# Performance work log

Measured on AMD Instinct MI355X. Metric: run time of the kernel, lower is better.

Reference implementation:

```python
import jax, jax.numpy as jnp
from jax import lax
import numpy as np

B, NW, L, E, H, V = 8192, 4, 16, 128, 128, 64  # batch, words/example, max chars, emsize, hidden, char vocab


def setup_inputs() -> dict:
    key = jax.random.key(0)
    ks = jax.random.split(key, 13)
    s = 0.05
    return {
        "word_ids": jax.random.randint(ks[0], (B, NW, L), 0, V, dtype=jnp.int32),
        "lengths": jax.random.randint(ks[1], (B, NW), 1, L + 1, dtype=jnp.int32),
        "emb_i": jax.random.normal(ks[2], (V, E), jnp.float32),
        "W_ih": jax.random.normal(ks[3], (4 * H, E), jnp.float32) * s,
        "W_hh": jax.random.normal(ks[4], (4 * H, H), jnp.float32) * s,
        "b_ih": jax.random.normal(ks[5], (4 * H,), jnp.float32) * s,
        "b_hh": jax.random.normal(ks[6], (4 * H,), jnp.float32) * s,
        "conv1_w": jax.random.normal(ks[7], (4, 1, 2, 2), jnp.float32) * 0.5,
        "conv1_b": jax.random.normal(ks[8], (4,), jnp.float32) * 0.1,
        "conv2_w": jax.random.normal(ks[9], (8, 4, 2, 2), jnp.float32) * 0.5,
        "conv2_b": jax.random.normal(ks[10], (8,), jnp.float32) * 0.1,
        "scorer_w": jax.random.normal(ks[11], (1, 2 * 2 * 8), jnp.float32) * 0.2,
        "scorer_b": jax.random.normal(ks[12], (1,), jnp.float32) * 0.1,
    }


def reference(word_ids, lengths, emb_i, W_ih, W_hh, b_ih, b_hh,
              conv1_w, conv1_b, conv2_w, conv2_b, scorer_w, scorer_b):
    Bx, NWx, Lx = word_ids.shape
    Hh = W_hh.shape[1]
    BN = Bx * NWx
    # char embeddings for all words, packed: [L, BN, E]
    xs = emb_i[word_ids.reshape(BN, Lx)].transpose(1, 0, 2)
    # ragged lengths -> per-step update mask [L, BN]
    mask = jnp.arange(Lx, dtype=lengths.dtype)[:, None] < lengths.reshape(-1)[None, :]
    h0 = jnp.zeros((BN, Hh), emb_i.dtype)

    def step(carry, xm):
        h, c = carry
        x_t, m = xm
        gates = x_t @ W_ih.T + b_ih + h @ W_hh.T + b_hh  # torch LSTMCell gate order i,f,g,o
        i, f, g, o = jnp.split(gates, 4, axis=-1)
        i = jax.nn.sigmoid(i); f = jax.nn.sigmoid(f)
        g = jnp.tanh(g); o = jax.nn.sigmoid(o)
        c_new = f * c + i * g
        h_new = o * jnp.tanh(c_new)
        m = m[:, None]
        return (jnp.where(m, h_new, h), jnp.where(m, c_new, c)), None

    (h, c), _ = lax.scan(step, (h0, h0), (xs, mask))
    # Model.encode returns the cell state c
    reps = c.reshape(Bx, NWx, Hh)

    # pairwise cosine similarity matrix [B, NW, NW]
    norms = jnp.sqrt(jnp.sum(reps * reps, axis=-1))
    dots = jnp.einsum('bih,bjh->bij', reps, reps)
    cos = dots / (norms[:, :, None] * norms[:, None, :])

    # tiny 2-layer CNN scorer on the NWxNW matrix (NCHW)
    dn = ('NCHW', 'OIHW', 'NCHW')
    x_img = cos[:, None, :, :]
    out = jax.nn.relu(lax.conv_general_dilated(x_img, conv1_w, (1, 1), 'VALID', dimension_numbers=dn)
                      + conv1_b[None, :, None, None])
    out = jax.nn.relu(lax.conv_general_dilated(out, conv2_w, (1, 1), 'VALID', dimension_numbers=dn)
                      + conv2_b[None, :, None, None])
    flat = out.reshape(Bx, -1)  # channel-major flatten matches torch .view
    score = flat @ scorer_w.T + scorer_b
    return jax.nn.sigmoid(score)  # [B, 1] discriminator prob
```

## Files before the change

kernel.cpp:

```cpp
#include <hip/hip_runtime.h>

#define BSZ    8192
#define NWRD   4
#define SEQL   16
#define HDIM   128
#define NSEQ   (BSZ * NWRD)
#define WGSEQ  32
#define UPB    80
#define BINCAP (UPB * WGSEQ)
#define NUNITS (16 * UPB)
#define HSTRIDE 136

typedef float  f32x4  __attribute__((ext_vector_type(4)));
typedef float  f32x16 __attribute__((ext_vector_type(16)));
typedef __bf16 bf16x8 __attribute__((ext_vector_type(8)));

union AccU { f32x16 v; f32x4 q[4]; float f[16]; };

__device__ __forceinline__ unsigned short f2bf(float f) {
    unsigned int u = __builtin_bit_cast(unsigned int, f);
    return (unsigned short)((u + 0x7fff + ((u >> 16) & 1)) >> 16);
}
__device__ __forceinline__ float sigm(float x) {
    return __builtin_amdgcn_rcpf(1.f + __builtin_amdgcn_exp2f(x * -1.44269504f));
}
__device__ __forceinline__ float tanhx(float x) {
    return 1.f - 2.f * __builtin_amdgcn_rcpf(1.f + __builtin_amdgcn_exp2f(x * 2.88539008f));
}

__global__ void prep4(const float* __restrict__ emb, const float* __restrict__ W_ih,
                      const float* __restrict__ b_ih, const float* __restrict__ b_hh,
                      const float* __restrict__ W_hh, const int* __restrict__ lengths,
                      float* __restrict__ P2T, unsigned short* __restrict__ WA,
                      int* __restrict__ perm, int* __restrict__ gh)
{
    __shared__ int lh[16], gbase[16];
    const int blk = blockIdx.x, tid = threadIdx.x;

    if (blk < 128) {
        int idx = blk * 256 + tid;
        int v = idx >> 9, g = (idx >> 7) & 3, j = idx & 127;
        int n = g * 128 + j;
        const f32x4* er = (const f32x4*)(emb  + v * 128);
        const f32x4* wr = (const f32x4*)(W_ih + n * 128);
        f32x4 s4 = er[0] * wr[0];
#pragma unroll
        for (int e = 1; e < 32; ++e) s4 += er[e] * wr[e];
        P2T[idx] = s4.x + s4.y + s4.z + s4.w + b_ih[n] + b_hh[n];
    } else if (blk < 384) {
        int idx = (blk - 128) * 256 + tid;
        int jj = idx & 7, lane = (idx >> 3) & 63, kc = (idx >> 9) & 7, tt = idx >> 12;
        int wv = tt >> 2, g = tt & 3;
        int n = g * 128 + wv * 32 + (lane & 31);
        int k = kc * 16 + (lane >> 5) * 8 + jj;
        WA[idx] = f2bf(W_hh[n * 128 + k]);
    } else {
        if (tid < 16) lh[tid] = 0;
        __syncthreads();
        int i = (blk - 384) * 256 + tid;
        int b = 16 - lengths[i];
        int rank = atomicAdd(&lh[b], 1);
        __syncthreads();
        if (tid < 16) gbase[tid] = atomicAdd(&gh[tid], lh[tid]);
        __syncthreads();
        perm[b * BINCAP + gbase[b] + rank] = i;
    }
}


#define GATE_PHASE(T, WRITE)                                                    \
    {                                                                           \
        const int wr_ = (WRITE);                                                \
        unsigned short* hw_ = hbuf[((T) + 1) & 1];                              \
        int wn_ = 0;                                                            \
        if (wr_) wn_ = words_s[lane31 * 17 + (T) + 1];                          \
        const char* pbn_ = P2c + ((size_t)wn_ << 11) + pboff;                   \
        _Pragma("unroll")                                                       \
        for (int q = 0; q < 4; ++q) {                                           \
            float hv_[4];                                                       \
            _Pragma("unroll")                                                   \
            for (int d = 0; d < 4; ++d) {                                       \
                const int r = q * 4 + d;                                        \
                float ig = sigm(acc[0].f[r]);                                   \
                float fg = sigm(acc[1].f[r]);                                   \
                float gg = tanhx(acc[2].f[r]);                                  \
                float cn = fg * cq[q][d] + ig * gg;                             \
                cq[q][d] = cn;                                                  \
                if (wr_) {                                                      \
                    float og = sigm(acc[3].f[r]);                               \
                    hv_[d] = og * tanhx(cn);                                    \
                }                                                               \
            }                                                                   \
            if (wr_) {                                                          \
                unsigned int plo_, phi_;                                        \
                asm("v_cvt_pk_bf16_f32 %0, %1, %2"                              \
                    : "=v"(plo_) : "v"(hv_[0]), "v"(hv_[1]));                   \
                asm("v_cvt_pk_bf16_f32 %0, %1, %2"                              \
                    : "=v"(phi_) : "v"(hv_[2]), "v"(hv_[3]));                   \
                unsigned long long pu_ =                                        \
                    ((unsigned long long)phi_ << 32) | plo_;                    \
                *(unsigned long long*)(hw_ + rdo + jbase + 8 * q) = pu_;        \
                             \
                _Pragma("unroll")                                               \
                for (int g = 0; g < 4; ++g)                                     \
                    acc[g].q[q] = *(const f32x4*)(pbn_ + g * 512 + q * 32);     \
            }                                                                   \
        }                                                                       \
    }

#define MFMA_STEP(T)                                                            \
    {                                                                           \
        const unsigned short* hr_ = hbuf[(T) & 1];                              \
        bf16x8 bfv_[8];                                                         \
        _Pragma("unroll")                                                       \
        for (int kc = 0; kc < 8; ++kc)                                          \
            bfv_[kc] = *(const bf16x8*)(hr_ + rdo + kc * 16 + hl * 8);          \
        _Pragma("unroll")                                                       \
        for (int kc = 0; kc < 8; ++kc) {                                        \
            const bf16x8 bb_ = bfv_[kc];                                        \
            _Pragma("unroll")                                                   \
            for (int g = 0; g < 4; ++g)                                         \
                acc[g].v = __builtin_amdgcn_mfma_f32_32x32x16_bf16(             \
                    afr[g][kc], bb_, acc[g].v, 0, 0, 0);                        \
        }                                                                       \
    }

__global__ __launch_bounds__(256, 2) void lstm4(
    const int* __restrict__ word_ids, const int* __restrict__ perm,
    const int* __restrict__ gh, const float* __restrict__ P2T,
    const unsigned short* __restrict__ WA, float* __restrict__ c_out)
{
    __shared__ __align__(16) unsigned short hbuf[2][WGSEQ * HSTRIDE];
    __shared__ int words_s[WGSEQ * 17];
    __shared__ int sid_s[WGSEQ];

    const int tid    = threadIdx.x;
    const int wv     = tid >> 6;
    const int lane   = tid & 63;
    const int lane31 = lane & 31;
    const int hl     = lane >> 5;

    const int u    = blockIdx.x;
    const int b    = u / UPB;
    const int widx = u % UPB;
    const int cnt  = gh[b];
    if (widx * WGSEQ >= cnt) return;
    const int ml   = 16 - b;

    if (tid < WGSEQ) {
        int slot = widx * WGSEQ + tid;
        sid_s[tid] = (slot < cnt) ? perm[b * BINCAP + slot] : 0;
    }
    __syncthreads();
    for (int i = tid; i < WGSEQ * SEQL; i += 256)
        words_s[(i >> 4) * 17 + (i & 15)] = word_ids[sid_s[i >> 4] * SEQL + (i & 15)];
    __syncthreads();

    bf16x8 afr[4][8];
#pragma unroll
    for (int g = 0; g < 4; ++g)
#pragma unroll
        for (int kc = 0; kc < 8; ++kc)
            afr[g][kc] = *(const bf16x8*)(WA + (((wv * 4 + g) * 8 + kc) * 64 + lane) * 8);

    f32x4 cq[4] = {{0,0,0,0},{0,0,0,0},{0,0,0,0},{0,0,0,0}};
    const char* P2c  = (const char*)P2T;
    const int pboff  = wv * 128 + hl * 16;
    const int rdo    = lane31 * HSTRIDE;
    const int jbase  = wv * 32 + 4 * hl;

    AccU acc[4];
    {
        const int w0 = words_s[lane31 * 17];
        const char* pb = P2c + ((size_t)w0 << 11) + pboff;
#pragma unroll
        for (int g = 0; g < 4; ++g)
#pragma unroll
            for (int q = 0; q < 4; ++q)
                acc[g].q[q] = *(const f32x4*)(pb + g * 512 + q * 32);
    }

    GATE_PHASE(0, ml > 1);
    if (ml > 1) {
        __syncthreads();
#pragma unroll 1
        for (int t = 1; t < ml - 1; ++t) {
            MFMA_STEP(t);
            GATE_PHASE(t, 1);
            __syncthreads();
        }
        MFMA_STEP(ml - 1);
        GATE_PHASE(ml - 1, 0);
    }

    if (widx * WGSEQ + lane31 < cnt) {
        const int sid = sid_s[lane31];
#pragma unroll
        for (int q = 0; q < 4; ++q)
            *(f32x4*)(c_out + sid * HDIM + jbase + 8 * q) = cq[q];
    }
}

__global__ __launch_bounds__(256) void epilogue(
    const float* __restrict__ c_ws,
    const float* __restrict__ conv1_w, const float* __restrict__ conv1_b,
    const float* __restrict__ conv2_w, const float* __restrict__ conv2_b,
    const float* __restrict__ scorer_w, const float* __restrict__ scorer_b,
    float* __restrict__ out)
{
    __shared__ __align__(16) float reps[8 * NWRD * HDIM];
    __shared__ float gram_s[8 * 16];

    const int tid = threadIdx.x;
    const int b0  = blockIdx.x * 8;

    for (int i = tid; i < 8 * NWRD * HDIM; i += 256)
        reps[i] = c_ws[b0 * NWRD * HDIM + i];
    __syncthreads();

    const int bt  = tid >> 5;
    const int sub = tid & 31;

    float dval = 0.f;
    if (sub < 16) {
        int i = sub >> 2, j = sub & 3;
        const f32x4* ci = (const f32x4*)(reps + (bt * 4 + i) * HDIM);
        const f32x4* cj = (const f32x4*)(reps + (bt * 4 + j) * HDIM);
        f32x4 s4 = {0.f, 0.f, 0.f, 0.f};
        for (int k = 0; k < HDIM / 4; ++k) s4 += ci[k] * cj[k];
        dval = s4.x + s4.y + s4.z + s4.w;
        gram_s[bt * 16 + sub] = dval;
    }
    __syncthreads();
    float cosv = 0.f;
    if (sub < 16) {
        int i = sub >> 2, j = sub & 3;
        float di = gram_s[bt * 16 + i * 4 + i];
        float dj = gram_s[bt * 16 + j * 4 + j];
        cosv = __fdividef(dval, sqrtf(di * dj));
    }
    __syncthreads();
    if (sub < 16) gram_s[bt * 16 + sub] = cosv;
    __syncthreads();

    if (sub == 0) {
        float img[4][4];
#pragma unroll
        for (int i = 0; i < 4; ++i)
#pragma unroll
            for (int j = 0; j < 4; ++j) img[i][j] = gram_s[bt * 16 + i * 4 + j];

        float o1[4][3][3];
#pragma unroll
        for (int ch = 0; ch < 4; ++ch) {
            float w00 = conv1_w[ch*4+0], w01 = conv1_w[ch*4+1];
            float w10 = conv1_w[ch*4+2], w11 = conv1_w[ch*4+3];
            float bb  = conv1_b[ch];
#pragma unroll
            for (int y = 0; y < 3; ++y)
#pragma unroll
                for (int x = 0; x < 3; ++x) {
                    float s = bb + w00*img[y][x]   + w01*img[y][x+1]
                                 + w10*img[y+1][x] + w11*img[y+1][x+1];
                    o1[ch][y][x] = s > 0.f ? s : 0.f;
                }
        }
        float sc = scorer_b[0];
#pragma unroll
        for (int oc = 0; oc < 8; ++oc) {
            float bb = conv2_b[oc];
#pragma unroll
            for (int y = 0; y < 2; ++y)
#pragma unroll
                for (int x = 0; x < 2; ++x) {
                    float s = bb;
#pragma unroll
                    for (int ic = 0; ic < 4; ++ic) {
                        const float* w = conv2_w + oc * 16 + ic * 4;
                        s += w[0]*o1[ic][y][x]   + w[1]*o1[ic][y][x+1]
                           + w[2]*o1[ic][y+1][x] + w[3]*o1[ic][y+1][x+1];
                    }
                    float rl = s > 0.f ? s : 0.f;
                    sc += rl * scorer_w[oc * 4 + y * 2 + x];
                }
        }
        out[blockIdx.x * 8 + bt] = sigm(sc);
    }
}

extern "C" void kernel_launch(void* const* d_in, const int* in_sizes, int n_in,
                              void* d_out, int out_size, void* d_ws, size_t ws_size,
                              hipStream_t stream)
{
    const int*   word_ids = (const int*)d_in[0];
    const int*   lengths  = (const int*)d_in[1];
    const float* emb      = (const float*)d_in[2];
    const float* W_ih     = (const float*)d_in[3];
    const float* W_hh     = (const float*)d_in[4];
    const float* b_ih     = (const float*)d_in[5];
    const float* b_hh     = (const float*)d_in[6];
    const float* conv1_w  = (const float*)d_in[7];
    const float* conv1_b  = (const float*)d_in[8];
    const float* conv2_w  = (const float*)d_in[9];
    const float* conv2_b  = (const float*)d_in[10];
    const float* scorer_w = (const float*)d_in[11];
    const float* scorer_b = (const float*)d_in[12];
    float* out = (float*)d_out;

    char* ws = (char*)d_ws;
    float*          P2T  = (float*)(ws + 0);
    unsigned short* WA   = (unsigned short*)(ws + (128<<10));
    int*            perm = (int*)(ws + (256<<10));
    int*            gh   = (int*)(ws + (416<<10));
    float*          c_ws = (float*)(ws + (512<<10));

    hipMemsetAsync(gh, 0, 16 * sizeof(int), stream);
    prep4   <<<512,   256, 0, stream>>>(emb, W_ih, b_ih, b_hh, W_hh, lengths,
                                        P2T, WA, perm, gh);
    lstm4   <<<NUNITS, 256, 0, stream>>>(word_ids, perm, gh, P2T, WA, c_ws);
    epilogue<<<BSZ / 8, 256, 0, stream>>>(c_ws, conv1_w, conv1_b, conv2_w, conv2_b,
                                          scorer_w, scorer_b, out);
}
```

Baseline: 194.0 us.

## Stage precomputed input projections into LDS via async global_load_lds

The per-step input-projection rows (P2T) are now prefetched one step ahead into a swizzled LDS buffer using global_load_lds, instead of each lane issuing global vector loads straight into accumulator registers. The h buffer drops from double to single buffering, and extra barriers order the LDS reads and writes. The goal is to take global-load latency off the recurrent critical path and cut VGPR pressure. In exchange the kernel uses 64KB more LDS per block, which may lower occupancy below the 2 blocks per CU requested, and adds a barrier per step.

```diff
diff --git a/kernel.cpp b/kernel.cpp
--- a/kernel.cpp
+++ b/kernel.cpp
@@ -10,6 +10,9 @@
 #define BINCAP (UPB * WGSEQ)
 #define NUNITS (16 * UPB)
 #define HSTRIDE 136
+
+#define AS1 __attribute__((address_space(1)))
+#define AS3 __attribute__((address_space(3)))
 
 typedef float  f32x4  __attribute__((ext_vector_type(4)));
 typedef float  f32x16 __attribute__((ext_vector_type(16)));
@@ -68,13 +71,54 @@
 }
 
 
-#define GATE_PHASE(T, WRITE)                                                    \
+#define LOAD_W(T)                                                               \
+    { _Pragma("unroll")                                                         \
+      for (int r_ = 0; r_ < 8; ++r_)                                            \
+          wreg[r_] = words_s[(wv * 8 + r_) * 17 + (T)]; }
+
+#define STAGE_P()                                                               \
+    { _Pragma("unroll")                                                         \
+      for (int r_ = 0; r_ < 8; ++r_) {                                          \
+          const int s_ = wv * 8 + r_;                                           \
+          const unsigned xv_ = (unsigned)((s_ & 7) << 4);                       \
+          const char* sb_ = (const char*)(P2T + ((size_t)wreg[r_] << 9));       \
+          float* db_ = pbuf + (s_ << 9);                                        \
+          __builtin_amdgcn_global_load_lds(                                     \
+              (const AS1 unsigned int*)(sb_ + ((unsigned)(lane << 4) ^ xv_)),   \
+              (AS3 unsigned int*)db_, 16, 0, 0);                                \
+          __builtin_amdgcn_global_load_lds(                                     \
+              (const AS1 unsigned int*)(sb_ + ((1024u + (unsigned)(lane << 4)) ^ xv_)), \
+              (AS3 unsigned int*)(db_ + 256), 16, 0, 0);                        \
+      } }
+
+#define LOAD_ACC()                                                              \
+    { const char* pr_ = (const char*)pbuf + (lane31 << 11);                     \
+      const unsigned xv_ = (unsigned)((lane31 & 7) << 4);                       \
+      _Pragma("unroll")                                                         \
+      for (int g = 0; g < 4; ++g)                                               \
+          _Pragma("unroll")                                                     \
+          for (int q = 0; q < 4; ++q)                                           \
+              acc[g].q[q] = *(const f32x4*)(pr_ +                               \
+                  (((unsigned)(g * 512 + q * 32 + pboff)) ^ xv_)); }
+
+#define LOAD_B()                                                                \
+    { _Pragma("unroll")                                                         \
+      for (int kc = 0; kc < 8; ++kc)                                            \
+          bfv[kc] = *(const bf16x8*)(hbuf + rdo + kc * 16 + hl * 8); }
+
+#define MFMA_ALL()                                                              \
+    { _Pragma("unroll")                                                         \
+      for (int kc = 0; kc < 8; ++kc) {                                          \
+          const bf16x8 bb_ = bfv[kc];                                           \
+          _Pragma("unroll")                                                     \
+          for (int g = 0; g < 4; ++g)                                           \
+              acc[g].v = __builtin_amdgcn_mfma_f32_32x32x16_bf16(               \
+                  afr[g][kc], bb_, acc[g].v, 0, 0, 0);                          \
+      } }
+
+#define GATE_PHASE(WRITE)                                                       \
     {                                                                           \
         const int wr_ = (WRITE);                                                \
-        unsigned short* hw_ = hbuf[((T) + 1) & 1];                              \
-        int wn_ = 0;                                                            \
-        if (wr_) wn_ = words_s[lane31 * 17 + (T) + 1];                          \
-        const char* pbn_ = P2c + ((size_t)wn_ << 11) + pboff;                   \
         _Pragma("unroll")                                                       \
         for (int q = 0; q < 4; ++q) {                                           \
             float hv_[4];                                                       \
@@ -99,29 +143,8 @@
                     : "=v"(phi_) : "v"(hv_[2]), "v"(hv_[3]));                   \
                 unsigned long long pu_ =                                        \
                     ((unsigned long long)phi_ << 32) | plo_;                    \
-                *(unsigned long long*)(hw_ + rdo + jbase + 8 * q) = pu_;        \
-                             \
-                _Pragma("unroll")                                               \
-                for (int g = 0; g < 4; ++g)                                     \
-                    acc[g].q[q] = *(const f32x4*)(pbn_ + g * 512 + q * 32);     \
+                *(unsigned long long*)(hbuf + rdo + jbase + 8 * q) = pu_;       \
             }                                                                   \
-        }                                                                       \
-    }
-
-#define MFMA_STEP(T)                                                            \
-    {                                                                           \
-        const unsigned short* hr_ = hbuf[(T) & 1];                              \
-        bf16x8 bfv_[8];                                                         \
-        _Pragma("unroll")                                                       \
-        for (int kc = 0; kc < 8; ++kc)                                          \
-            bfv_[kc] = *(const bf16x8*)(hr_ + rdo + kc * 16 + hl * 8);          \
-        _Pragma("unroll")                                                       \
-        for (int kc = 0; kc < 8; ++kc) {                                        \
-            const bf16x8 bb_ = bfv_[kc];                                        \
-            _Pragma("unroll")                                                   \
-            for (int g = 0; g < 4; ++g)                                         \
-                acc[g].v = __builtin_amdgcn_mfma_f32_32x32x16_bf16(             \
-                    afr[g][kc], bb_, acc[g].v, 0, 0, 0);                        \
         }                                                                       \
     }
 
@@ -130,7 +153,8 @@
     const int* __restrict__ gh, const float* __restrict__ P2T,
     const unsigned short* __restrict__ WA, float* __restrict__ c_out)
 {
-    __shared__ __align__(16) unsigned short hbuf[2][WGSEQ * HSTRIDE];
+    __shared__ __align__(16) float pbuf[WGSEQ * 512];
+    __shared__ __align__(16) unsigned short hbuf[WGSEQ * HSTRIDE];
     __shared__ int words_s[WGSEQ * 17];
     __shared__ int sid_s[WGSEQ];
 
@@ -147,6 +171,13 @@
     if (widx * WGSEQ >= cnt) return;
     const int ml   = 16 - b;
 
+    bf16x8 afr[4][8];
+#pragma unroll
+    for (int g = 0; g < 4; ++g)
+#pragma unroll
+        for (int kc = 0; kc < 8; ++kc)
+            afr[g][kc] = *(const bf16x8*)(WA + (((wv * 4 + g) * 8 + kc) * 64 + lane) * 8);
+
     if (tid < WGSEQ) {
         int slot = widx * WGSEQ + tid;
         sid_s[tid] = (slot < cnt) ? perm[b * BINCAP + slot] : 0;
@@ -156,41 +187,43 @@
         words_s[(i >> 4) * 17 + (i & 15)] = word_ids[sid_s[i >> 4] * SEQL + (i & 15)];
     __syncthreads();
 
-    bf16x8 afr[4][8];
-#pragma unroll
-    for (int g = 0; g < 4; ++g)
-#pragma unroll
-        for (int kc = 0; kc < 8; ++kc)
-            afr[g][kc] = *(const bf16x8*)(WA + (((wv * 4 + g) * 8 + kc) * 64 + lane) * 8);
-
     f32x4 cq[4] = {{0,0,0,0},{0,0,0,0},{0,0,0,0},{0,0,0,0}};
-    const char* P2c  = (const char*)P2T;
-    const int pboff  = wv * 128 + hl * 16;
-    const int rdo    = lane31 * HSTRIDE;
-    const int jbase  = wv * 32 + 4 * hl;
+    const int pboff = wv * 128 + hl * 16;
+    const int rdo   = lane31 * HSTRIDE;
+    const int jbase = wv * 32 + 4 * hl;
+    int wreg[8];
+
+    LOAD_W(0);
+    STAGE_P();
+    __syncthreads();
 
     AccU acc[4];
-    {
-        const int w0 = words_s[lane31 * 17];
-        const char* pb = P2c + ((size_t)w0 << 11) + pboff;
-#pragma unroll
-        for (int g = 0; g < 4; ++g)
-#pragma unroll
-            for (int q = 0; q < 4; ++q)
-                acc[g].q[q] = *(const f32x4*)(pb + g * 512 + q * 32);
-    }
-
-    GATE_PHASE(0, ml > 1);
+    LOAD_ACC();
     if (ml > 1) {
         __syncthreads();
+        LOAD_W(1);
+        STAGE_P();
+    }
+    GATE_PHASE(ml > 1);
+
+    if (ml > 1) {
+        __syncthreads();
+        bf16x8 bfv[8];
 #pragma unroll 1
         for (int t = 1; t < ml - 1; ++t) {
-            MFMA_STEP(t);
-            GATE_PHASE(t, 1);
+            LOAD_B();
+            LOAD_ACC();
+            LOAD_W(t + 1);
+            __syncthreads();
+            STAGE_P();
+            MFMA_ALL();
+            GATE_PHASE(1);
             __syncthreads();
         }
-        MFMA_STEP(ml - 1);
-        GATE_PHASE(ml - 1, 0);
+        LOAD_B();
+        LOAD_ACC();
+        MFMA_ALL();
+        GATE_PHASE(0);
     }
 
     if (widx * WGSEQ + lane31 < cnt) {
```

Result: faster. 184.7 us (-4.8%).
